# Performance work log

Hardware: AMD Instinct MI355X
Metric: run time of the kernel (lower is better)

The kernel has to match this reference:

```python
import jax, jax.numpy as jnp
import numpy as np

EMBED_DIM = 1024
NUM_HEADS = 16
HEAD_DIM = EMBED_DIM // NUM_HEADS
T_Q = 2048
T_K = 2048
B = 4
NEG_INF = -1e9


def setup_inputs() -> dict:
    key = jax.random.key(0)
    ks = jax.random.split(key, 8)
    q = jax.random.normal(ks[0], (T_Q, B, EMBED_DIM), dtype=jnp.float32)
    k = jax.random.normal(ks[1], (T_K, B, EMBED_DIM), dtype=jnp.float32)
    v = jax.random.normal(ks[2], (T_K, B, EMBED_DIM), dtype=jnp.float32)
    # True = padded key position (masked out)
    key_padding_mask = jax.random.randint(ks[3], (B, T_K), 0, 2).astype(jnp.bool_)
    # torch nn.Linear weights: shape (out, in), y = x @ W^T
    scale = 1.0 / np.sqrt(EMBED_DIM)
    Wq = jax.random.uniform(ks[4], (EMBED_DIM, EMBED_DIM), jnp.float32, -scale, scale)
    Wk = jax.random.uniform(ks[5], (EMBED_DIM, EMBED_DIM), jnp.float32, -scale, scale)
    Wv = jax.random.uniform(ks[6], (EMBED_DIM, EMBED_DIM), jnp.float32, -scale, scale)
    Wo = jax.random.uniform(ks[7], (EMBED_DIM, EMBED_DIM), jnp.float32, -scale, scale)
    return {"q": q, "k": k, "v": v, "key_padding_mask": key_padding_mask,
            "Wq": Wq, "Wk": Wk, "Wv": Wv, "Wo": Wo}


def _proj_split(W, x):
    # x: (T, B, E), W: (E, E) torch layout -> (B, H, T, d_k)
    T = x.shape[0]
    y = jnp.einsum('tbe,fe->tbf', x, W)
    return y.reshape(T, B, NUM_HEADS, HEAD_DIM).transpose(1, 2, 0, 3)


def reference(q, k, v, key_padding_mask, Wq, Wk, Wv, Wo):
    Q = _proj_split(Wq, q)  # (B, H, T_q, d_k)
    K = _proj_split(Wk, k)  # (B, H, T_k, d_k)
    V = _proj_split(Wv, v)  # (B, H, T_k, d_k)
    scores = jnp.einsum('bhqd,bhkd->bhqk', Q, K) / jnp.sqrt(
        jnp.asarray(HEAD_DIM, dtype=Q.dtype))
    scores = jnp.where(key_padding_mask[:, None, None, :], NEG_INF, scores)
    attn = jax.nn.softmax(scores, axis=-1)  # dropout p=0.0 -> identity
    out = jnp.einsum('bhqk,bhkd->bhqd', attn, V)  # (B, H, T_q, d_k)
    out = out.transpose(2, 0, 1, 3).reshape(q.shape[0], q.shape[1], EMBED_DIM)
    return jnp.einsum('tbe,fe->tbf', out, Wo)
```

## Files before the change

kernel.cpp:

```cpp
#include <hip/hip_runtime.h>
#include <stdint.h>

#define TSEQ 2048
#define NB   4
#define NH   16
#define HD   64
#define EMB  1024
#define ROWS (TSEQ*NB)
#define NKT  (EMB/64)
#define PREP_BLOCKS 28672

typedef __attribute__((ext_vector_type(8))) short bf16x8;
typedef __attribute__((ext_vector_type(4))) short bf16x4;
typedef __attribute__((ext_vector_type(4))) float f32x4;

__device__ __forceinline__ short f2bf(float x) {
    uint32_t u = __builtin_bit_cast(uint32_t, x);
    u += 0x7fffu + ((u >> 16) & 1u);
    return (short)(u >> 16);
}

__device__ __forceinline__ uint32_t pack2bf(float a, float b) {
    uint32_t ua = __builtin_bit_cast(uint32_t, a) + 0x8000u;
    uint32_t ub = __builtin_bit_cast(uint32_t, b) + 0x8000u;
    return (ua >> 16) | (ub & 0xffff0000u);
}

__device__ __forceinline__ void gld16(const void* g, void* l) {
    __builtin_amdgcn_global_load_lds(
        (const __attribute__((address_space(1))) void*)g,
        (__attribute__((address_space(3))) void*)l,
        16, 0, 0);
}

__global__ __launch_bounds__(256)
void prep_scan(const float* __restrict__ q, const float* __restrict__ k, const float* __restrict__ v,
               const float* __restrict__ Wq, const float* __restrict__ Wk,
               const float* __restrict__ Wv, const float* __restrict__ Wo,
               short* __restrict__ Wbf,
               short* __restrict__ Xq, short* __restrict__ Xk, short* __restrict__ Xv,
               const int* __restrict__ mask, int* __restrict__ idxc, int* __restrict__ inv,
               float* __restrict__ bias_c, int* __restrict__ npad)
{
    __shared__ int sums[256];
    __shared__ int totalv;
    const int bid = blockIdx.x, tid = threadIdx.x;

    if (bid < PREP_BLOCKS) {
        int gid = bid * 256 + tid;
        const float4* s4;
        bf16x4* d4;
        if (gid < (1 << 20)) {
            int wsel = gid >> 18;
            const float* src = (wsel == 0) ? Wq : (wsel == 1) ? Wk : (wsel == 2) ? Wv : Wo;
            s4 = (const float4*)src + (gid & ((1 << 18) - 1));
            d4 = (bf16x4*)Wbf + gid;
        } else {
            int iid = gid - (1 << 20);
            int isel = iid >> 21, o = iid & ((1 << 21) - 1);
            const float* src = (isel == 0) ? q : (isel == 1) ? k : v;
            short* dst = (isel == 0) ? Xq : (isel == 1) ? Xk : Xv;
            s4 = (const float4*)src + o;
            d4 = (bf16x4*)dst + o;
        }
        float4 vv = *s4;
        bf16x4 o4 = { f2bf(vv.x), f2bf(vv.y), f2bf(vv.z), f2bf(vv.w) };
        *d4 = o4;
        return;
    }

    const int b = bid - PREP_BLOCKS;
    const int* mb = mask + b * TSEQ;
    int valid[8]; int cnt = 0;
    #pragma unroll
    for (int j = 0; j < 8; j++) { valid[j] = (mb[tid * 8 + j] == 0); cnt += valid[j]; }
    sums[tid] = cnt;
    __syncthreads();
    for (int off = 1; off < 256; off <<= 1) {
        int vv = (tid >= off) ? sums[tid - off] : 0;
        __syncthreads();
        sums[tid] += vv;
        __syncthreads();
    }
    if (tid == 255) totalv = sums[255];
    int base = sums[tid] - cnt;
    __syncthreads();
    int nv = totalv;
    #pragma unroll
    for (int j = 0; j < 8; j++) {
        int t = tid * 8 + j;
        if (valid[j]) { idxc[b * TSEQ + base] = t; inv[b * TSEQ + t] = base; base++; }
        else          { inv[b * TSEQ + t] = -1; }
    }
    for (int i = tid; i < TSEQ; i += 256) {
        if (i >= nv) idxc[b * TSEQ + i] = 0;
        bias_c[b * TSEQ + i] = (i < nv) ? -12.0f : -1e9f;
    }
    if (tid == 0) npad[b] = (nv + 63) & ~63;
}


#define DSA(MH)                                                                     \
    _Pragma("unroll")                                                               \
    for (int mf = 0; mf < 4; mf++) {                                                \
        _Pragma("unroll")                                                           \
        for (int ks = 0; ks < 2; ks++) {                                            \
            const int rr = wm*64 + mf*16 + c;                                       \
            const int cb = (ks*64 + g*16) ^ ((rr & 7) << 4);                        \
            af[mf][ks] = *(const bf16x8*)(&lds[cur][0][MH][0] + rr*64 + (cb >> 1)); \
        }                                                                           \
    }

#define DSB(NH_, DST)                                                               \
    _Pragma("unroll")                                                               \
    for (int nf = 0; nf < 2; nf++) {                                                \
        _Pragma("unroll")                                                           \
        for (int ks = 0; ks < 2; ks++) {                                            \
            const int rr = wn*32 + nf*16 + c;                                       \
            const int cb = (ks*64 + g*16) ^ ((rr & 7) << 4);                        \
            DST[nf][ks] = *(const bf16x8*)(&lds[cur][1][NH_][0] + rr*64 + (cb >> 1));\
        }                                                                           \
    }

#define MM(MH, NH_, BREG)                                                           \
    __builtin_amdgcn_s_barrier();                                                   \
    asm volatile("s_waitcnt lgkmcnt(0)" ::: "memory");                              \
    __builtin_amdgcn_sched_barrier(0);                                              \
    __builtin_amdgcn_s_setprio(1);                                                  \
    _Pragma("unroll")                                                               \
    for (int mf = 0; mf < 4; mf++) {                                                \
        _Pragma("unroll")                                                           \
        for (int nf = 0; nf < 2; nf++) {                                            \
            acc[MH][NH_][mf][nf] = __builtin_amdgcn_mfma_f32_16x16x32_bf16(         \
                af[mf][0], BREG[nf][0], acc[MH][NH_][mf][nf], 0, 0, 0);             \
            acc[MH][NH_][mf][nf] = __builtin_amdgcn_mfma_f32_16x16x32_bf16(         \
                af[mf][1], BREG[nf][1], acc[MH][NH_][mf][nf], 0, 0, 0);             \
        }                                                                           \
    }                                                                               \
    __builtin_amdgcn_s_setprio(0);                                                  \
    __builtin_amdgcn_sched_barrier(0);

__global__ __launch_bounds__(512, 2)
void proj_gemm8(const short* __restrict__ Xq, const short* __restrict__ Xk, const short* __restrict__ Xv,
                const short* __restrict__ Wbf, const int* __restrict__ inv,
                short* __restrict__ Qw, short* __restrict__ Kc, short* __restrict__ Vw)
{
    __shared__ __align__(16) short lds[2][2][2][128*64];
    const int z = blockIdx.z;
    const short* __restrict__ A  = (z == 0) ? Xq : (z == 1) ? Xk : Xv;
    const short* __restrict__ Bw = Wbf + (size_t)z * (EMB*EMB);
    short* __restrict__ dst = (z == 0) ? Qw : (z == 1) ? Kc : Vw;
    const float scale = (z == 0) ? 0.18033688011112042f : 1.0f;

    const int tid = threadIdx.x;
    const int lane = tid & 63, w = tid >> 6;
    const int wm = w >> 2, wn = w & 3;
    const int g = lane >> 4, c = lane & 15;
    const int m0 = blockIdx.x * 256, n0 = blockIdx.y * 256;

    const short* a0 = A  + (size_t)m0 * EMB;
    const short* a1 = a0 + (size_t)128 * EMB;
    const short* b0 = Bw + (size_t)n0 * EMB;
    const short* b1 = b0 + (size_t)128 * EMB;

    auto stage = [&](const short* grow, short* lhalf) {
        #pragma unroll
        for (int p = 0; p < 2; p++) {
            const int lin = p * 8192 + w * 1024 + lane * 16;
            const int rin = lin >> 7;
            const int cb  = (lin & 127) ^ ((rin & 7) << 4);
            gld16(grow + (size_t)rin * EMB + (cb >> 1), lhalf + p * 4096 + w * 512);
        }
    };

    stage(a0,      &lds[0][0][0][0]);
    stage(a1,      &lds[0][0][1][0]);
    stage(b0,      &lds[0][1][0][0]);
    stage(b1,      &lds[0][1][1][0]);
    stage(a0 + 64, &lds[1][0][0][0]);
    stage(b0 + 64, &lds[1][1][0][0]);
    asm volatile("s_waitcnt vmcnt(4)" ::: "memory");
    __builtin_amdgcn_s_barrier();

    f32x4 acc[2][2][4][2] = {};

    #pragma unroll 2
    for (int t = 0; t < NKT; t++) {
        const int cur = t & 1, nxt = cur ^ 1;
        const int k1 = (t + 1 < NKT ? t + 1 : NKT - 1) * 64;
        const int k2 = (t + 2 < NKT ? t + 2 : NKT - 1) * 64;
        bf16x8 af[4][2], b0r[2][2], b1r[2][2];
        DSA(0); DSB(0, b0r);
        stage(a1 + k1, &lds[nxt][0][1][0]);
        MM(0, 0, b0r)
        __builtin_amdgcn_s_barrier();
        DSB(1, b1r);
        stage(b1 + k1, &lds[nxt][1][1][0]);
        MM(0, 1, b1r)
        __builtin_amdgcn_s_barrier();
        DSA(1);
        stage(a0 + k2, &lds[cur][0][0][0]);
        MM(1, 1, b1r)
        __builtin_amdgcn_s_barrier();
        stage(b0 + k2, &lds[cur][1][0][0]);
        MM(1, 0, b0r)
        asm volatile("s_waitcnt vmcnt(4)" ::: "memory");
        __builtin_amdgcn_s_barrier();
    }
    asm volatile("s_waitcnt vmcnt(0)" ::: "memory");

    if (z == 1) {
        #pragma unroll
        for (int mh = 0; mh < 2; mh++)
            #pragma unroll
            for (int nh = 0; nh < 2; nh++)
                #pragma unroll
                for (int mf = 0; mf < 4; mf++)
                    #pragma unroll
                    for (int nf = 0; nf < 2; nf++)
                        #pragma unroll
                        for (int r = 0; r < 4; r++) {
                            int row = m0 + mh*128 + wm*64 + mf*16 + g*4 + r;
                            int col = n0 + nh*128 + wn*32 + nf*16 + c;
                            int tq = row >> 2, bb = row & 3, h = col >> 6, dk = col & 63;
                            int i = inv[bb * TSEQ + tq];
                            if (i >= 0)
                                dst[(((size_t)(bb*16 + h) * TSEQ + i) << 6) + dk]
                                    = f2bf(acc[mh][nh][mf][nf][r]);
                        }
    } else {
        #pragma unroll
        for (int mh = 0; mh < 2; mh++)
            #pragma unroll
            for (int nh = 0; nh < 2; nh++)
                #pragma unroll
                for (int mf = 0; mf < 4; mf++)
                    #pragma unroll
                    for (int nf = 0; nf < 2; nf++)
                        #pragma unroll
                        for (int r = 0; r < 4; r++) {
                            int row = m0 + mh*128 + wm*64 + mf*16 + g*4 + r;
                            int col = n0 + nh*128 + wn*32 + nf*16 + c;
                            int tq = row >> 2, bb = row & 3, h = col >> 6, dk = col & 63;
                            dst[(((size_t)(bb*16 + h) * TSEQ + tq) << 6) + dk]
                                = f2bf(acc[mh][nh][mf][nf][r] * scale);
                        }
    }
}

__global__ __launch_bounds__(256)
void gather_v(const short* __restrict__ V,
              const int* __restrict__ idxc, const int* __restrict__ npad,
              short* __restrict__ Vtc)
{
    const int bh = blockIdx.y, b = bh >> 4;
    const int i0 = blockIdx.x * 64;
    if (i0 >= npad[b]) return;
    __shared__ __align__(16) short tile[64*72];
    __shared__ int sidx[64];
    const int tid = threadIdx.x;
    if (tid < 64) sidx[tid] = idxc[b * TSEQ + i0 + tid];
    __syncthreads();
    const short* __restrict__ Vh = V + (size_t)bh * TSEQ * HD;
    #pragma unroll
    for (int p = 0; p < 2; p++) {
        int idx = tid + p * 256, row = idx >> 3, cc = idx & 7;
        int src = sidx[row];
        *(int4*)(&tile[row * 72 + cc * 8]) = *(const int4*)(Vh + (size_t)src * HD + cc * 8);
    }
    __syncthreads();
    #pragma unroll
    for (int p = 0; p < 2; p++) {
        int idx = tid + p * 256, dv = idx >> 3, cc = idx & 7;
        bf16x8 o;
        #pragma unroll
        for (int j = 0; j < 8; j++) o[j] = tile[(cc * 8 + j) * 72 + dv];
        *(bf16x8*)(Vtc + ((size_t)bh * HD + dv) * TSEQ + i0 + cc * 8) = o;
    }
}

__global__ __launch_bounds__(256, 3)
void attn_kernel(const short* __restrict__ Q, const short* __restrict__ K,
                 const short* __restrict__ Vt, const float* __restrict__ bias,
                 const int* __restrict__ npad,
                 short* __restrict__ O)
{
    __shared__ __align__(16) short Ks [64*72];
    __shared__ __align__(16) short Vts[64*72];
    __shared__ __align__(16) short Ps [128*72];
    __shared__ __align__(16) float bias_lds[64];

    const int bh = blockIdx.y;
    const int b_ = bh >> 4, h_ = bh & 15;
    const int q0 = blockIdx.x * 128;
    const int tid = threadIdx.x, lane = tid & 63, wv = tid >> 6;
    const int g = lane >> 4, c = lane & 15;
    const int qb = wv * 32;
    const short* __restrict__ Qh  = Q  + (size_t)bh * TSEQ * HD;
    const short* __restrict__ Kh  = K  + (size_t)bh * TSEQ * HD;
    const short* __restrict__ Vth = Vt + (size_t)bh * HD * TSEQ;
    const float* __restrict__ biasb = bias + b_ * TSEQ;
    const int nit = npad[b_] >> 6;

    const int srow = tid >> 3, scc = tid & 7;

    *(int4*)(&Ks [ srow       * 72 + scc * 8]) = *(const int4*)(Kh  + (size_t) srow       * HD + scc * 8);
    *(int4*)(&Ks [(srow + 32) * 72 + scc * 8]) = *(const int4*)(Kh  + (size_t)(srow + 32) * HD + scc * 8);
    *(int4*)(&Vts[ srow       * 72 + scc * 8]) = *(const int4*)(Vth + (size_t) srow       * TSEQ + scc * 8);
    *(int4*)(&Vts[(srow + 32) * 72 + scc * 8]) = *(const int4*)(Vth + (size_t)(srow + 32) * TSEQ + scc * 8);
    if (tid < 16) ((float4*)bias_lds)[tid] = ((const float4*)biasb)[tid];

    bf16x8 qf[2][2];
    #pragma unroll
    for (int j = 0; j < 2; j++)
        #pragma unroll
        for (int ks = 0; ks < 2; ks++)
            qf[j][ks] = *(const bf16x8*)(Qh + (size_t)(q0 + qb + j * 16 + c) * HD + ks * 32 + g * 8);
    __syncthreads();

    float lacc[2] = { 0.0f, 0.0f };
    f32x4 oacc[2][4] = {};

    for (int it = 0; it < nit; it++) {
        f32x4 sacc[2][4];
        #pragma unroll
        for (int mt = 0; mt < 4; mt++) {
            f32x4 bv = *(const f32x4*)(&bias_lds[mt * 16 + g * 4]);
            sacc[0][mt] = bv; sacc[1][mt] = bv;
        }

        int4 kr0, kr1, vr0, vr1; float4 br;
        const bool pfv = (it + 1 < nit);
        if (pfv) {
            int tk0n = (it + 1) * 64;
            kr0 = *(const int4*)(Kh  + (size_t)(tk0n + srow)      * HD + scc * 8);
            kr1 = *(const int4*)(Kh  + (size_t)(tk0n + srow + 32) * HD + scc * 8);
            vr0 = *(const int4*)(Vth + (size_t) srow       * TSEQ + tk0n + scc * 8);
            vr1 = *(const int4*)(Vth + (size_t)(srow + 32) * TSEQ + tk0n + scc * 8);
            if (tid < 16) br = ((const float4*)(biasb + tk0n))[tid];
        }

        __builtin_amdgcn_s_setprio(1);
        #pragma unroll
        for (int ks = 0; ks < 2; ks++)
            #pragma unroll
            for (int mt = 0; mt < 4; mt++) {
                bf16x8 kf = *(const bf16x8*)(&Ks[(mt * 16 + c) * 72 + ks * 32 + g * 8]);
                sacc[0][mt] = __builtin_amdgcn_mfma_f32_16x16x32_bf16(kf, qf[0][ks], sacc[0][mt], 0, 0, 0);
                sacc[1][mt] = __builtin_amdgcn_mfma_f32_16x16x32_bf16(kf, qf[1][ks], sacc[1][mt], 0, 0, 0);
            }
        __builtin_amdgcn_s_setprio(0);

        #pragma unroll
        for (int j = 0; j < 2; j++) {
            int prow = (qb + j * 16 + c) * 72;
            float lp = 0.0f;
            #pragma unroll
            for (int mt = 0; mt < 4; mt++) {
                float e0 = __builtin_amdgcn_exp2f(sacc[j][mt][0]);
                float e1 = __builtin_amdgcn_exp2f(sacc[j][mt][1]);
                float e2 = __builtin_amdgcn_exp2f(sacc[j][mt][2]);
                float e3 = __builtin_amdgcn_exp2f(sacc[j][mt][3]);
                lp += (e0 + e1) + (e2 + e3);
                uint2 pw = { pack2bf(e0, e1), pack2bf(e2, e3) };
                *(uint2*)(&Ps[prow + mt * 16 + g * 4]) = pw;
            }
            lacc[j] += lp;
        }
        __builtin_amdgcn_sched_barrier(0);

        __builtin_amdgcn_s_setprio(1);
        #pragma unroll
        for (int s2 = 0; s2 < 2; s2++) {
            bf16x8 pf0 = *(const bf16x8*)(&Ps[(qb +      c) * 72 + s2 * 32 + g * 8]);
            bf16x8 pf1 = *(const bf16x8*)(&Ps[(qb + 16 + c) * 72 + s2 * 32 + g * 8]);
            #pragma unroll
            for (int mtv = 0; mtv < 4; mtv++) {
                bf16x8 vf = *(const bf16x8*)(&Vts[(mtv * 16 + c) * 72 + s2 * 32 + g * 8]);
                oacc[0][mtv] = __builtin_amdgcn_mfma_f32_16x16x32_bf16(vf, pf0, oacc[0][mtv], 0, 0, 0);
                oacc[1][mtv] = __builtin_amdgcn_mfma_f32_16x16x32_bf16(vf, pf1, oacc[1][mtv], 0, 0, 0);
            }
        }
        __builtin_amdgcn_s_setprio(0);

        if (pfv) {
            __syncthreads();
            *(int4*)(&Ks [ srow       * 72 + scc * 8]) = kr0;
            *(int4*)(&Ks [(srow + 32) * 72 + scc * 8]) = kr1;
            *(int4*)(&Vts[ srow       * 72 + scc * 8]) = vr0;
            *(int4*)(&Vts[(srow + 32) * 72 + scc * 8]) = vr1;
            if (tid < 16) ((float4*)bias_lds)[tid] = br;
            __syncthreads();
        }
    }

    __syncthreads();
    #pragma unroll
    for (int j = 0; j < 2; j++) {
        float l = lacc[j];
        l += __shfl_xor(l, 16);
        l += __shfl_xor(l, 32);
        float inv_ = 1.0f / l;
        int orow = (qb + j * 16 + c) * 72;
        #pragma unroll
        for (int mtv = 0; mtv < 4; mtv++) {
            uint2 ow = { pack2bf(oacc[j][mtv][0] * inv_, oacc[j][mtv][1] * inv_),
                         pack2bf(oacc[j][mtv][2] * inv_, oacc[j][mtv][3] * inv_) };
            *(uint2*)(&Ps[orow + mtv * 16 + g * 4]) = ow;
        }
    }
    __syncthreads();
    #pragma unroll
    for (int i = 0; i < 4; i++) {
        int idx = tid + i * 256, row = idx >> 3, cc = idx & 7;
        *(int4*)(O + (((size_t)(q0 + row) * NB + b_) << 10) + h_ * 64 + cc * 8)
            = *(const int4*)(&Ps[row * 72 + cc * 8]);
    }
}

__global__ __launch_bounds__(256, 2)
void out_gemm(const short* __restrict__ A, const short* __restrict__ Bw, float* __restrict__ C)
{
    __shared__ __align__(16) short As[128*32];
    __shared__ __align__(16) short Bs[128*32];
    const int tid = threadIdx.x;
    const int lane = tid & 63, w = tid >> 6;
    const int wm = w >> 1, wn = w & 1;
    const int g = lane >> 4, c = lane & 15;
    const int m0 = blockIdx.x * 128, n0 = blockIdx.y * 128;

    const int l4 = lane >> 2, col8 = (lane & 3) * 8;
    const short* gA = A  + (size_t)(m0 + w*16 + l4) * EMB + col8;
    const short* gB = Bw + (size_t)(n0 + w*16 + l4) * EMB + col8;
    short* ldsA0 = &As[(w*16) * 32];
    short* ldsA1 = &As[(64 + w*16) * 32];
    short* ldsB0 = &Bs[(w*16) * 32];
    short* ldsB1 = &Bs[(64 + w*16) * 32];

    f32x4 acc[4][4] = {};
    for (int kt = 0; kt < EMB; kt += 32) {
        gld16(gA + kt,          ldsA0);
        gld16(gA + 64*EMB + kt, ldsA1);
        gld16(gB + kt,          ldsB0);
        gld16(gB + 64*EMB + kt, ldsB1);
        __syncthreads();
        bf16x8 a[4], b[4];
        #pragma unroll
        for (int mt = 0; mt < 4; mt++) a[mt] = *(const bf16x8*)(&As[(wm*64 + mt*16 + c) * 32 + g * 8]);
        #pragma unroll
        for (int nt = 0; nt < 4; nt++) b[nt] = *(const bf16x8*)(&Bs[(wn*64 + nt*16 + c) * 32 + g * 8]);
        #pragma unroll
        for (int mt = 0; mt < 4; mt++)
            #pragma unroll
            for (int nt = 0; nt < 4; nt++)
                acc[mt][nt] = __builtin_amdgcn_mfma_f32_16x16x32_bf16(a[mt], b[nt], acc[mt][nt], 0, 0, 0);
        __syncthreads();
    }
    #pragma unroll
    for (int mt = 0; mt < 4; mt++)
        #pragma unroll
        for (int nt = 0; nt < 4; nt++)
            #pragma unroll
            for (int r = 0; r < 4; r++) {
                int row = m0 + wm*64 + mt*16 + g*4 + r;
                int col = n0 + wn*64 + nt*16 + c;
                C[(size_t)row * EMB + col] = acc[mt][nt][r];
            }
}

extern "C" void kernel_launch(void* const* d_in, const int* in_sizes, int n_in,
                              void* d_out, int out_size, void* d_ws, size_t ws_size,
                              hipStream_t stream)
{
    const float* q    = (const float*)d_in[0];
    const float* k    = (const float*)d_in[1];
    const float* v    = (const float*)d_in[2];
    const int*   mask = (const int*)  d_in[3];
    const float* Wq   = (const float*)d_in[4];
    const float* Wk   = (const float*)d_in[5];
    const float* Wv   = (const float*)d_in[6];
    const float* Wo   = (const float*)d_in[7];
    float* out = (float*)d_out;

    char* ws = (char*)d_ws;
    short* Wbf    = (short*)(ws);
    short* Qws    = (short*)(ws +  8388608);
    short* Kc     = (short*)(ws + 25165824);
    short* Vws    = (short*)(ws + 41943040);
    short* Vtc    = (short*)(ws + 58720256);
    short* Ows    = (short*)(ws + 75497472);
    float* bias_c = (float*)(ws + 92274688);
    short* Xvbf   = (short*)(ws + 92307456);
    int*   idxc   = (int*)  (ws + 109084672);
    int*   npad   = (int*)  (ws + 109117440);
    int*   inv    = (int*)  (ws + 109117504);
    short* Xqbf = Ows;
    short* Xkbf = Vtc;

    prep_scan<<<PREP_BLOCKS + NB, 256, 0, stream>>>(q, k, v, Wq, Wk, Wv, Wo,
                                                    Wbf, Xqbf, Xkbf, Xvbf,
                                                    mask, idxc, inv, bias_c, npad);
    proj_gemm8<<<dim3(ROWS/256, EMB/256, 3), 512, 0, stream>>>(Xqbf, Xkbf, Xvbf, Wbf, inv,
                                                               Qws, Kc, Vws);
    gather_v<<<dim3(TSEQ/64, NB*NH), 256, 0, stream>>>(Vws, idxc, npad, Vtc);
    attn_kernel<<<dim3(TSEQ/128, NB*NH), 256, 0, stream>>>(Qws, Kc, Vtc, bias_c, npad, Ows);
    out_gemm<<<dim3(ROWS/128, EMB/128), 256, 0, stream>>>(Ows, Wbf + (size_t)3*EMB*EMB, out);
}
```

Before: 306.8 us.

## Compact K/V rows before projection and skip padded-row projection tiles

Key-padding compaction moves before the projection: the mask scan becomes its own kernel, and the fp32-to-bf16 conversion of k and v gathers only the valid key rows into a batch-major compacted layout, zero-filling the rest. The K and V projection blocks whose row tile lies entirely past the padded valid count now exit early, and gather_v reads contiguous rows instead of indexed ones. The aim is to cut the projection GEMM work for K and V roughly in proportion to the masked fraction and to drop the inverse-index scatter. In exchange there is an extra kernel launch and a serial dependency of the conversion on the scan.

New measurement: 308.8 us. About the same (+0.7%).

```diff
diff --git a/kernel.cpp b/kernel.cpp
--- a/kernel.cpp
+++ b/kernel.cpp
@@ -34,42 +34,12 @@
 }
 
 __global__ __launch_bounds__(256)
-void prep_scan(const float* __restrict__ q, const float* __restrict__ k, const float* __restrict__ v,
-               const float* __restrict__ Wq, const float* __restrict__ Wk,
-               const float* __restrict__ Wv, const float* __restrict__ Wo,
-               short* __restrict__ Wbf,
-               short* __restrict__ Xq, short* __restrict__ Xk, short* __restrict__ Xv,
-               const int* __restrict__ mask, int* __restrict__ idxc, int* __restrict__ inv,
-               float* __restrict__ bias_c, int* __restrict__ npad)
-{
+void scan_kernel(const int* __restrict__ mask, int* __restrict__ idxc,
+                 float* __restrict__ bias_c, int* __restrict__ npad)
+{
+    const int b = blockIdx.x, tid = threadIdx.x;
     __shared__ int sums[256];
     __shared__ int totalv;
-    const int bid = blockIdx.x, tid = threadIdx.x;
-
-    if (bid < PREP_BLOCKS) {
-        int gid = bid * 256 + tid;
-        const float4* s4;
-        bf16x4* d4;
-        if (gid < (1 << 20)) {
-            int wsel = gid >> 18;
-            const float* src = (wsel == 0) ? Wq : (wsel == 1) ? Wk : (wsel == 2) ? Wv : Wo;
-            s4 = (const float4*)src + (gid & ((1 << 18) - 1));
-            d4 = (bf16x4*)Wbf + gid;
-        } else {
-            int iid = gid - (1 << 20);
-            int isel = iid >> 21, o = iid & ((1 << 21) - 1);
-            const float* src = (isel == 0) ? q : (isel == 1) ? k : v;
-            short* dst = (isel == 0) ? Xq : (isel == 1) ? Xk : Xv;
-            s4 = (const float4*)src + o;
-            d4 = (bf16x4*)dst + o;
-        }
-        float4 vv = *s4;
-        bf16x4 o4 = { f2bf(vv.x), f2bf(vv.y), f2bf(vv.z), f2bf(vv.w) };
-        *d4 = o4;
-        return;
-    }
-
-    const int b = bid - PREP_BLOCKS;
     const int* mb = mask + b * TSEQ;
     int valid[8]; int cnt = 0;
     #pragma unroll
@@ -87,16 +57,51 @@
     __syncthreads();
     int nv = totalv;
     #pragma unroll
-    for (int j = 0; j < 8; j++) {
-        int t = tid * 8 + j;
-        if (valid[j]) { idxc[b * TSEQ + base] = t; inv[b * TSEQ + t] = base; base++; }
-        else          { inv[b * TSEQ + t] = -1; }
-    }
+    for (int j = 0; j < 8; j++)
+        if (valid[j]) { idxc[b * TSEQ + base] = tid * 8 + j; base++; }
     for (int i = tid; i < TSEQ; i += 256) {
         if (i >= nv) idxc[b * TSEQ + i] = 0;
         bias_c[b * TSEQ + i] = (i < nv) ? -12.0f : -1e9f;
     }
-    if (tid == 0) npad[b] = (nv + 63) & ~63;
+    if (tid == 0) { npad[b] = (nv + 63) & ~63; npad[4 + b] = nv; }
+}
+
+__global__ __launch_bounds__(256)
+void prep_kernel(const float* __restrict__ q, const float* __restrict__ k, const float* __restrict__ v,
+                 const float* __restrict__ Wq, const float* __restrict__ Wk,
+                 const float* __restrict__ Wv, const float* __restrict__ Wo,
+                 short* __restrict__ Wbf,
+                 short* __restrict__ Xq, short* __restrict__ Xkc, short* __restrict__ Xvc,
+                 const int* __restrict__ idxc, const int* __restrict__ npad)
+{
+    int gid = blockIdx.x * 256 + threadIdx.x;
+    if (gid < (1 << 20)) {
+        int wsel = gid >> 18;
+        const float* src = (wsel == 0) ? Wq : (wsel == 1) ? Wk : (wsel == 2) ? Wv : Wo;
+        float4 vv = ((const float4*)src)[gid & ((1 << 18) - 1)];
+        bf16x4 o4 = { f2bf(vv.x), f2bf(vv.y), f2bf(vv.z), f2bf(vv.w) };
+        ((bf16x4*)Wbf)[gid] = o4;
+        return;
+    }
+    int iid = gid - (1 << 20);
+    int isel = iid >> 21, o = iid & ((1 << 21) - 1);
+    if (isel == 0) {
+        float4 vv = ((const float4*)q)[o];
+        bf16x4 o4 = { f2bf(vv.x), f2bf(vv.y), f2bf(vv.z), f2bf(vv.w) };
+        ((bf16x4*)Xq)[o] = o4;
+    } else {
+        const float* src = (isel == 1) ? k : v;
+        short* dst = (isel == 1) ? Xkc : Xvc;
+        int row = o >> 8, col4 = o & 255;
+        int b = row >> 11, i = row & 2047;
+        bf16x4 o4 = { 0, 0, 0, 0 };
+        if (i < npad[4 + b]) {
+            int t = idxc[b * TSEQ + i];
+            float4 vv = ((const float4*)src)[((size_t)(t * NB + b) << 8) + col4];
+            o4 = bf16x4{ f2bf(vv.x), f2bf(vv.y), f2bf(vv.z), f2bf(vv.w) };
+        }
+        ((bf16x4*)dst)[o] = o4;
+    }
 }
 
 
@@ -141,13 +146,16 @@
     __builtin_amdgcn_sched_barrier(0);
 
 __global__ __launch_bounds__(512, 2)
-void proj_gemm8(const short* __restrict__ Xq, const short* __restrict__ Xk, const short* __restrict__ Xv,
-                const short* __restrict__ Wbf, const int* __restrict__ inv,
+void proj_gemm8(const short* __restrict__ Xq, const short* __restrict__ Xkc, const short* __restrict__ Xvc,
+                const short* __restrict__ Wbf, const int* __restrict__ npad,
                 short* __restrict__ Qw, short* __restrict__ Kc, short* __restrict__ Vw)
 {
+    const int z = blockIdx.z;
+    const int m0 = blockIdx.x * 256, n0 = blockIdx.y * 256;
+    if (z != 0 && (m0 & 2047) >= npad[m0 >> 11]) return;
+
     __shared__ __align__(16) short lds[2][2][2][128*64];
-    const int z = blockIdx.z;
-    const short* __restrict__ A  = (z == 0) ? Xq : (z == 1) ? Xk : Xv;
+    const short* __restrict__ A  = (z == 0) ? Xq : (z == 1) ? Xkc : Xvc;
     const short* __restrict__ Bw = Wbf + (size_t)z * (EMB*EMB);
     short* __restrict__ dst = (z == 0) ? Qw : (z == 1) ? Kc : Vw;
     const float scale = (z == 0) ? 0.18033688011112042f : 1.0f;
@@ -156,7 +164,6 @@
     const int lane = tid & 63, w = tid >> 6;
     const int wm = w >> 2, wn = w & 3;
     const int g = lane >> 4, c = lane & 15;
-    const int m0 = blockIdx.x * 256, n0 = blockIdx.y * 256;
 
     const short* a0 = A  + (size_t)m0 * EMB;
     const short* a1 = a0 + (size_t)128 * EMB;
@@ -209,26 +216,7 @@
     }
     asm volatile("s_waitcnt vmcnt(0)" ::: "memory");
 
-    if (z == 1) {
-        #pragma unroll
-        for (int mh = 0; mh < 2; mh++)
-            #pragma unroll
-            for (int nh = 0; nh < 2; nh++)
-                #pragma unroll
-                for (int mf = 0; mf < 4; mf++)
-                    #pragma unroll
-                    for (int nf = 0; nf < 2; nf++)
-                        #pragma unroll
-                        for (int r = 0; r < 4; r++) {
-                            int row = m0 + mh*128 + wm*64 + mf*16 + g*4 + r;
-                            int col = n0 + nh*128 + wn*32 + nf*16 + c;
-                            int tq = row >> 2, bb = row & 3, h = col >> 6, dk = col & 63;
-                            int i = inv[bb * TSEQ + tq];
-                            if (i >= 0)
-                                dst[(((size_t)(bb*16 + h) * TSEQ + i) << 6) + dk]
-                                    = f2bf(acc[mh][nh][mf][nf][r]);
-                        }
-    } else {
+    if (z == 0) {
         #pragma unroll
         for (int mh = 0; mh < 2; mh++)
             #pragma unroll
@@ -245,28 +233,40 @@
                             dst[(((size_t)(bb*16 + h) * TSEQ + tq) << 6) + dk]
                                 = f2bf(acc[mh][nh][mf][nf][r] * scale);
                         }
+    } else {
+        #pragma unroll
+        for (int mh = 0; mh < 2; mh++)
+            #pragma unroll
+            for (int nh = 0; nh < 2; nh++)
+                #pragma unroll
+                for (int mf = 0; mf < 4; mf++)
+                    #pragma unroll
+                    for (int nf = 0; nf < 2; nf++)
+                        #pragma unroll
+                        for (int r = 0; r < 4; r++) {
+                            int row = m0 + mh*128 + wm*64 + mf*16 + g*4 + r;
+                            int col = n0 + nh*128 + wn*32 + nf*16 + c;
+                            int i = row & 2047, bb = row >> 11, h = col >> 6, dk = col & 63;
+                            dst[(((size_t)(bb*16 + h) * TSEQ + i) << 6) + dk]
+                                = f2bf(acc[mh][nh][mf][nf][r]);
+                        }
     }
 }
 
 __global__ __launch_bounds__(256)
-void gather_v(const short* __restrict__ V,
-              const int* __restrict__ idxc, const int* __restrict__ npad,
+void gather_v(const short* __restrict__ V, const int* __restrict__ npad,
               short* __restrict__ Vtc)
 {
     const int bh = blockIdx.y, b = bh >> 4;
     const int i0 = blockIdx.x * 64;
     if (i0 >= npad[b]) return;
     __shared__ __align__(16) short tile[64*72];
-    __shared__ int sidx[64];
     const int tid = threadIdx.x;
-    if (tid < 64) sidx[tid] = idxc[b * TSEQ + i0 + tid];
-    __syncthreads();
     const short* __restrict__ Vh = V + (size_t)bh * TSEQ * HD;
     #pragma unroll
     for (int p = 0; p < 2; p++) {
         int idx = tid + p * 256, row = idx >> 3, cc = idx & 7;
-        int src = sidx[row];
-        *(int4*)(&tile[row * 72 + cc * 8]) = *(const int4*)(Vh + (size_t)src * HD + cc * 8);
+        *(int4*)(&tile[row * 72 + cc * 8]) = *(const int4*)(Vh + (size_t)(i0 + row) * HD + cc * 8);
     }
     __syncthreads();
     #pragma unroll
@@ -493,16 +493,15 @@
     short* Xvbf   = (short*)(ws + 92307456);
     int*   idxc   = (int*)  (ws + 109084672);
     int*   npad   = (int*)  (ws + 109117440);
-    int*   inv    = (int*)  (ws + 109117504);
     short* Xqbf = Ows;
     short* Xkbf = Vtc;
 
-    prep_scan<<<PREP_BLOCKS + NB, 256, 0, stream>>>(q, k, v, Wq, Wk, Wv, Wo,
-                                                    Wbf, Xqbf, Xkbf, Xvbf,
-                                                    mask, idxc, inv, bias_c, npad);
-    proj_gemm8<<<dim3(ROWS/256, EMB/256, 3), 512, 0, stream>>>(Xqbf, Xkbf, Xvbf, Wbf, inv,
+    scan_kernel<<<NB, 256, 0, stream>>>(mask, idxc, bias_c, npad);
+    prep_kernel<<<PREP_BLOCKS, 256, 0, stream>>>(q, k, v, Wq, Wk, Wv, Wo,
+                                                 Wbf, Xqbf, Xkbf, Xvbf, idxc, npad);
+    proj_gemm8<<<dim3(ROWS/256, EMB/256, 3), 512, 0, stream>>>(Xqbf, Xkbf, Xvbf, Wbf, npad,
                                                                Qws, Kc, Vws);
-    gather_v<<<dim3(TSEQ/64, NB*NH), 256, 0, stream>>>(Vws, idxc, npad, Vtc);
+    gather_v<<<dim3(TSEQ/64, NB*NH), 256, 0, stream>>>(Vws, npad, Vtc);
     attn_kernel<<<dim3(TSEQ/128, NB*NH), 256, 0, stream>>>(Qws, Kc, Vtc, bias_c, npad, Ows);
     out_gemm<<<dim3(ROWS/128, EMB/128), 256, 0, stream>>>(Ows, Wbf + (size_t)3*EMB*EMB, out);
 }
```
